# Performance work log

Hardware: AMD Instinct MI355X
Metric: run time of the kernel (lower is better)

Reference implementation:

```python
import jax, jax.numpy as jnp
import numpy as np
import math

BLOCK_SIZE = 512

def _block_attention(query, key, value):
    # query/key/value: [B, S, H, D]; block-wise attention with PER-BLOCK softmax
    # and normalizer accumulation, faithful to _ring_attention_single (causal, no dropout).
    B, S, H, D = query.shape
    bs = BLOCK_SIZE
    nb = S // bs
    scale = 1.0 / math.sqrt(D)
    neg = jnp.where(jnp.triu(jnp.ones((bs, bs), dtype=bool), 1), -jnp.inf, 0.0)  # strict-upper causal mask for diagonal block
    outs = []
    for i in range(nb):  # small fixed number of blocks (8)
        qb = query[:, i * bs:(i + 1) * bs]                      # [B, bs, H, D]
        kb = key[:, :(i + 1) * bs]                              # [B, (i+1)*bs, H, D]
        vb = value[:, :(i + 1) * bs].reshape(B, i + 1, bs, H, D)
        s = jnp.einsum('bqhd,bkhd->bhqk', qb, kb) * scale       # [B, H, bs, (i+1)*bs]
        s = s.reshape(B, H, bs, i + 1, bs)
        s = s.at[:, :, :, i, :].add(neg)                        # causal mask on diagonal block j == i
        p = jax.nn.softmax(s, axis=-1)                          # softmax PER kv block (faithful to source)
        o = jnp.einsum('bhqjk,bjkhd->bqhd', p, vb)              # accumulated block outputs
        norm = p.sum(axis=-1).sum(axis=-1)                      # [B, H, bs] accumulated normalizer (== i+1 per row)
        norm = jnp.clip(norm, 1e-6, None).transpose(0, 2, 1)[..., None]  # [B, bs, H, 1]
        outs.append(o / norm)
    return jnp.concatenate(outs, axis=1)  # [B, S, H, D]


def setup_inputs() -> dict:
    key = jax.random.key(0)
    k1, k2, k3 = jax.random.split(key, 3)
    shape = (2, 4096, 16, 128)
    return {
        'query': jax.random.normal(k1, shape, dtype=jnp.float32),
        'key': jax.random.normal(k2, shape, dtype=jnp.float32),
        'value': jax.random.normal(k3, shape, dtype=jnp.float32),
    }


def reference(query, key, value):
    return _block_attention(query, key, value)
```

## Files before the change

### kernel.cpp

```cpp
#include <hip/hip_runtime.h>

typedef short bf16x8 __attribute__((ext_vector_type(8)));
typedef short bf16x4 __attribute__((ext_vector_type(4)));
typedef float f32x4  __attribute__((ext_vector_type(4)));
typedef float f32x16 __attribute__((ext_vector_type(16)));
typedef unsigned int u32;
typedef u32 u32x4 __attribute__((ext_vector_type(4)));

#define SEQ 4096
#define NH  16
#define HD  128

__device__ __forceinline__ short bf16_rne(float x) {
  u32 u = __builtin_bit_cast(u32, x);
  u = (u + 0x7FFFu + ((u >> 16) & 1u)) >> 16;
  return (short)u;
}

typedef __attribute__((address_space(1))) const void as1c_void;
typedef __attribute__((address_space(3))) void as3_void;

#define CVTPK(d, a, b) asm("v_cvt_pk_bf16_f32 %0, %1, %2" : "=v"(d) : "v"(a), "v"(b))
#define PLSWAP(x, y)   asm("v_permlane32_swap_b32 %0, %1" : "+v"(x), "+v"(y))

__global__ __launch_bounds__(256) void prep_k(const float* __restrict__ K,
                                              short* __restrict__ Kp) {
  int idx = blockIdx.x * 256 + threadIdx.x;
  int d4 = idx & 31;
  int s  = (idx >> 5) & 4095;
  int h  = (idx >> 17) & 15;
  int b  = idx >> 21;
  f32x4 v = *(const f32x4*)(K + (((size_t)(b * SEQ + s) * NH + h) << 7) + d4 * 4);
  bf16x4 o;
  o[0] = bf16_rne(v[0]); o[1] = bf16_rne(v[1]);
  o[2] = bf16_rne(v[2]); o[3] = bf16_rne(v[3]);
  int x = (d4 * 4) ^ ((s & 7) << 3);
  *(bf16x4*)(Kp + (((size_t)(b * NH + h) * SEQ + s) << 7) + x) = o;
}

__global__ __launch_bounds__(256) void prep_v(const float* __restrict__ V,
                                              short* __restrict__ Vt) {
  __shared__ short tile[64 * 128];
  int bid = blockIdx.x;
  int sb = bid & 63;
  int h  = (bid >> 6) & 15;
  int b  = bid >> 10;
  int t = threadIdx.x;
  {
    int s = t >> 2;
    int dbase = (t & 3) * 32;
    const float* src = V + (((size_t)(b * SEQ + sb * 64 + s) * NH + h) << 7) + dbase;
    int sw = (s & 7) << 3;
#pragma unroll
    for (int j = 0; j < 8; ++j) {
      f32x4 v = *(const f32x4*)(src + j * 4);
      bf16x4 o;
      o[0] = bf16_rne(v[0]); o[1] = bf16_rne(v[1]);
      o[2] = bf16_rne(v[2]); o[3] = bf16_rne(v[3]);
      int d = dbase + j * 4;
      *(bf16x4*)&tile[s * 128 + (d ^ sw)] = o;
    }
  }
  __syncthreads();
  {
    int w = t >> 6, l = t & 63, g = l >> 4, lq = l & 15;
    int srel = lq * 4;
#pragma unroll
    for (int j = 0; j < 8; ++j) {
      int d = w * 32 + j * 4 + g;
      bf16x4 o;
#pragma unroll
      for (int i = 0; i < 4; ++i) {
        int s = srel + i;
        o[i] = tile[s * 128 + (d ^ ((s & 7) << 3))];
      }
      int sp = srel ^ ((d & 7) << 3);
      *(bf16x4*)(Vt + (((size_t)(b * NH + h) * HD + d) << 12) + sb * 64 + sp) = o;
    }
  }
}

__global__ __launch_bounds__(256, 2) void attn_main(const float* __restrict__ Q,
                                                    const short* __restrict__ Kp,
                                                    const short* __restrict__ Vt,
                                                    float* __restrict__ Out) {
  __shared__ __align__(16) short sK[2][64 * 128];
  __shared__ __align__(16) short sV[2][128 * 64];

  int bid0 = (int)blockIdx.x;
  int bid = (bid0 & 7) * 64 + (bid0 >> 3);
  int p  = bid & 15;
  int h  = (bid >> 4) & 15;
  int b  = bid >> 8;

  int tid = threadIdx.x;
  int l = tid & 63, w = tid >> 6;
  int q5 = l & 31;
  int hi = l >> 5;
  int hi4 = hi * 4, hi8 = hi * 8;
  int cswz = (l & 7) << 4;

  int kcol[8], vcol[4];
#pragma unroll
  for (int i = 0; i < 8; ++i) kcol[i] = (i * 32 + hi * 16) ^ cswz;
#pragma unroll
  for (int ks = 0; ks < 4; ++ks) vcol[ks] = (ks * 32 + hi * 16) ^ cswz;

  const int pat[16] = {0,1,2,3, 8,9,10,11, 16,17,18,19, 24,25,26,27};

  const char* KbB = (const char*)(Kp + ((size_t)(b * NH + h) << 19));
  const char* VbB = (const char*)(Vt + ((size_t)(b * NH + h) << 19));

  const char* kgb[4]; const char* vgb[4]; int ldo[4];
#pragma unroll
  for (int j = 0; j < 4; ++j) {
    int idx = j * 256 + tid;
    kgb[j] = KbB + idx * 16;
    vgb[j] = VbB + (size_t)(idx >> 3) * 8192 + (idx & 7) * 16;
    ldo[j] = idx * 16;
  }

  const float SCL = 0.08838834764831845f * 1.4426950408889634f;

  for (int ts = 0; ts < 2; ++ts) {
    int qt = ts ? p : (31 - p);
    int iblk = qt >> 2;
    int qrow0 = qt * 128 + w * 32;
    int qg = qrow0 + q5;
    int qgrel = (qt & 3) * 128 + w * 32 + q5;
    int nch_w = (qt & 3) * 2 + (w >> 1) + 1;
    int ntot = 8 * iblk + (qt & 3) * 2 + 2;

    bf16x8 qf[8];
    {
      const float* qp = Q + (((size_t)(b * SEQ + qg) * NH + h) << 7);
#pragma unroll
      for (int i = 0; i < 8; ++i) {
        int d0 = i * 16 + hi8;
        f32x4 a = *(const f32x4*)(qp + d0);
        f32x4 c2 = *(const f32x4*)(qp + d0 + 4);
        bf16x8 f;
        f[0] = bf16_rne(a[0] * SCL);  f[1] = bf16_rne(a[1] * SCL);
        f[2] = bf16_rne(a[2] * SCL);  f[3] = bf16_rne(a[3] * SCL);
        f[4] = bf16_rne(c2[0] * SCL); f[5] = bf16_rne(c2[1] * SCL);
        f[6] = bf16_rne(c2[2] * SCL); f[7] = bf16_rne(c2[3] * SCL);
        qf[i] = f;
      }
    }

    f32x16 ot[4], ob[4];
#pragma unroll
    for (int dt = 0; dt < 4; ++dt) {
#pragma unroll
      for (int r = 0; r < 16; ++r) { ot[dt][r] = 0.f; ob[dt][r] = 0.f; }
    }
    float Z = 0.0f;

    __syncthreads();
#pragma unroll
    for (int j = 0; j < 4; ++j) {
      __builtin_amdgcn_global_load_lds((as1c_void*)kgb[j], (as3_void*)((char*)sK[0] + ldo[j]), 16, 0, 0);
      __builtin_amdgcn_global_load_lds((as1c_void*)vgb[j], (as3_void*)((char*)sV[0] + ldo[j]), 16, 0, 0);
    }

#pragma unroll 2
    for (int t = 0; t < ntot; ++t) {
      __syncthreads();

      int bi = (t + 1) & 1;
      if (t + 1 < ntot) {
#pragma unroll
        for (int j = 0; j < 4; ++j) {
          __builtin_amdgcn_global_load_lds((as1c_void*)(kgb[j] + (size_t)(t + 1) * 16384),
                                           (as3_void*)((char*)sK[bi] + ldo[j]), 16, 0, 0);
          __builtin_amdgcn_global_load_lds((as1c_void*)(vgb[j] + (size_t)(t + 1) * 128),
                                           (as3_void*)((char*)sV[bi] + ldo[j]), 16, 0, 0);
        }
      }

      int jb = t >> 3, c = t & 7;
      const int diag = (jb == iblk);

      if (!(diag && c >= nch_w)) {
        const char* kbuf = (const char*)sK[t & 1];
        const char* vbuf = (const char*)sV[t & 1];
        float csum = 0.0f;

        f32x16 st0, st1;
#pragma unroll
        for (int r = 0; r < 16; ++r) { st0[r] = 0.f; st1[r] = 0.f; }
        int rowb = q5 * 256;
        __builtin_amdgcn_s_setprio(1);
#pragma unroll
        for (int i = 0; i < 8; ++i) {
          bf16x8 kf0 = *(const bf16x8*)(kbuf + rowb + kcol[i]);
          bf16x8 kf1 = *(const bf16x8*)(kbuf + 8192 + rowb + kcol[i]);
          st0 = __builtin_amdgcn_mfma_f32_32x32x16_bf16(kf0, qf[i], st0, 0, 0, 0);
          st1 = __builtin_amdgcn_mfma_f32_32x32x16_bf16(kf1, qf[i], st1, 0, 0, 0);
        }
        __builtin_amdgcn_s_setprio(0);

        if (diag && c == nch_w - 1) {
          int lim0 = qgrel - c * 64;
          int lim1 = lim0 - 32;
#pragma unroll
          for (int r = 0; r < 16; ++r) {
            int pr4 = pat[r] + hi4;
            if (pr4 > lim0) st0[r] = -1e30f;
            if (pr4 > lim1) st1[r] = -1e30f;
          }
        }

        bf16x8 pa0, pa1, pa2, pa3;
        {
          float pr[16];
#pragma unroll
          for (int r = 0; r < 16; ++r) {
            pr[r] = __builtin_amdgcn_exp2f(st0[r]);
            csum += pr[r];
          }
          u32 X0, X1, Y0, Y1, A0, A1, B0, B1;
          CVTPK(X0, pr[0], pr[1]);   CVTPK(X1, pr[2], pr[3]);
          CVTPK(Y0, pr[4], pr[5]);   CVTPK(Y1, pr[6], pr[7]);
          PLSWAP(X0, Y0); PLSWAP(X1, Y1);
          pa0 = __builtin_bit_cast(bf16x8, (u32x4){X0, X1, Y0, Y1});
          CVTPK(A0, pr[8], pr[9]);   CVTPK(A1, pr[10], pr[11]);
          CVTPK(B0, pr[12], pr[13]); CVTPK(B1, pr[14], pr[15]);
          PLSWAP(A0, B0); PLSWAP(A1, B1);
          pa1 = __builtin_bit_cast(bf16x8, (u32x4){A0, A1, B0, B1});
        }
        __builtin_amdgcn_s_setprio(1);
#pragma unroll
        for (int dt = 0; dt < 4; ++dt) {
          bf16x8 vf = *(const bf16x8*)(vbuf + (dt * 32 + q5) * 128 + vcol[0]);
          ob[dt] = __builtin_amdgcn_mfma_f32_32x32x16_bf16(pa0, vf, ob[dt], 0, 0, 0);
        }
#pragma unroll
        for (int dt = 0; dt < 4; ++dt) {
          bf16x8 vf = *(const bf16x8*)(vbuf + (dt * 32 + q5) * 128 + vcol[1]);
          ob[dt] = __builtin_amdgcn_mfma_f32_32x32x16_bf16(pa1, vf, ob[dt], 0, 0, 0);
        }
        __builtin_amdgcn_s_setprio(0);

        {
          float pr[16];
#pragma unroll
          for (int r = 0; r < 16; ++r) {
            pr[r] = __builtin_amdgcn_exp2f(st1[r]);
            csum += pr[r];
          }
          u32 X0, X1, Y0, Y1, A0, A1, B0, B1;
          CVTPK(X0, pr[0], pr[1]);   CVTPK(X1, pr[2], pr[3]);
          CVTPK(Y0, pr[4], pr[5]);   CVTPK(Y1, pr[6], pr[7]);
          PLSWAP(X0, Y0); PLSWAP(X1, Y1);
          pa2 = __builtin_bit_cast(bf16x8, (u32x4){X0, X1, Y0, Y1});
          CVTPK(A0, pr[8], pr[9]);   CVTPK(A1, pr[10], pr[11]);
          CVTPK(B0, pr[12], pr[13]); CVTPK(B1, pr[14], pr[15]);
          PLSWAP(A0, B0); PLSWAP(A1, B1);
          pa3 = __builtin_bit_cast(bf16x8, (u32x4){A0, A1, B0, B1});
        }
        __builtin_amdgcn_s_setprio(1);
#pragma unroll
        for (int dt = 0; dt < 4; ++dt) {
          bf16x8 vf = *(const bf16x8*)(vbuf + (dt * 32 + q5) * 128 + vcol[2]);
          ob[dt] = __builtin_amdgcn_mfma_f32_32x32x16_bf16(pa2, vf, ob[dt], 0, 0, 0);
        }
#pragma unroll
        for (int dt = 0; dt < 4; ++dt) {
          bf16x8 vf = *(const bf16x8*)(vbuf + (dt * 32 + q5) * 128 + vcol[3]);
          ob[dt] = __builtin_amdgcn_mfma_f32_32x32x16_bf16(pa3, vf, ob[dt], 0, 0, 0);
        }
        __builtin_amdgcn_s_setprio(0);

        Z += csum;
      }

      if ((t & 7) == 7 || t == ntot - 1) {
        float zf = Z + __shfl_xor(Z, 32, 64);
        float rzL = 1.0f / zf;
        float rz[16];
#pragma unroll
        for (int r = 0; r < 16; ++r) rz[r] = __shfl(rzL, pat[r] + hi4, 64);
#pragma unroll
        for (int dt = 0; dt < 4; ++dt) {
#pragma unroll
          for (int r = 0; r < 16; ++r) {
            ot[dt][r] += ob[dt][r] * rz[r];
            ob[dt][r] = 0.f;
          }
        }
        Z = 0.0f;
      }
    }

    float rnorm = 1.0f / (float)(iblk + 1);
#pragma unroll
    for (int dt = 0; dt < 4; ++dt) {
#pragma unroll
      for (int r = 0; r < 16; ++r) {
        int qrow = qrow0 + pat[r] + hi4;
        Out[(((size_t)(b * SEQ + qrow) * NH + h) << 7) + dt * 32 + q5] = ot[dt][r] * rnorm;
      }
    }
  }
}

extern "C" void kernel_launch(void* const* d_in, const int* in_sizes, int n_in,
                              void* d_out, int out_size, void* d_ws, size_t ws_size,
                              hipStream_t stream) {
  const float* Q = (const float*)d_in[0];
  const float* K = (const float*)d_in[1];
  const float* V = (const float*)d_in[2];
  float* out = (float*)d_out;

  short* Kp = (short*)d_ws;
  short* Vt = Kp + (size_t)2 * NH * SEQ * HD;

  prep_k<<<(2 * NH * SEQ * (HD / 4)) / 256, 256, 0, stream>>>(K, Kp);
  prep_v<<<2 * NH * (SEQ / 64), 256, 0, stream>>>(V, Vt);
  attn_main<<<2 * NH * 16, 256, 0, stream>>>(Q, Kp, Vt, out);
}
```

Baseline: 206.6 us.

## Software-pipeline PV of previous tile with QK of current tile

Restructures the KV loop so each iteration runs the QK^T MFMAs for the current tile, then the P·V MFMAs for the previous tile's probabilities, then the softmax/exp for the current tile. This interleaves independent matrix work with exp and conversion work to hide latency. V staging becomes triple-buffered so the previous tile's V stays resident while the next one loads, and the block-normalizer fold is deferred to follow the matching PV. In exchange it raises LDS use to 80 KB per block and register pressure, since the probability fragments are carried across iterations, and it drops the unroll-2 pragma.

```diff
diff --git a/kernel.cpp b/kernel.cpp
--- a/kernel.cpp
+++ b/kernel.cpp
@@ -85,7 +85,7 @@
                                                     const short* __restrict__ Vt,
                                                     float* __restrict__ Out) {
   __shared__ __align__(16) short sK[2][64 * 128];
-  __shared__ __align__(16) short sV[2][128 * 64];
+  __shared__ __align__(16) short sV[3][128 * 64];
 
   int bid0 = (int)blockIdx.x;
   int bid = (bid0 & 7) * 64 + (bid0 >> 3);
@@ -156,51 +156,98 @@
     }
     float Z = 0.0f;
 
+    char* kcur = (char*)&sK[0][0]; char* knxt = (char*)&sK[1][0];
+    char* vcur = (char*)&sV[0][0]; char* vnxt = (char*)&sV[1][0]; char* vfre = (char*)&sV[2][0];
+
     __syncthreads();
 #pragma unroll
     for (int j = 0; j < 4; ++j) {
-      __builtin_amdgcn_global_load_lds((as1c_void*)kgb[j], (as3_void*)((char*)sK[0] + ldo[j]), 16, 0, 0);
-      __builtin_amdgcn_global_load_lds((as1c_void*)vgb[j], (as3_void*)((char*)sV[0] + ldo[j]), 16, 0, 0);
-    }
-
-#pragma unroll 2
+      __builtin_amdgcn_global_load_lds((as1c_void*)kgb[j], (as3_void*)(kcur + ldo[j]), 16, 0, 0);
+      __builtin_amdgcn_global_load_lds((as1c_void*)vgb[j], (as3_void*)(vcur + ldo[j]), 16, 0, 0);
+    }
+
+    bf16x8 pa0p, pa1p, pa2p, pa3p;
+    const char* pvb = vcur;
+    int havepa = 0, foldafter = 0;
+    f32x16 st0, st1;
+
+    auto QK = [&]() {
+#pragma unroll
+      for (int r = 0; r < 16; ++r) { st0[r] = 0.f; st1[r] = 0.f; }
+      int rowb = q5 * 256;
+      __builtin_amdgcn_s_setprio(1);
+#pragma unroll
+      for (int i = 0; i < 8; ++i) {
+        bf16x8 kf0 = *(const bf16x8*)(kcur + rowb + kcol[i]);
+        bf16x8 kf1 = *(const bf16x8*)(kcur + 8192 + rowb + kcol[i]);
+        st0 = __builtin_amdgcn_mfma_f32_32x32x16_bf16(kf0, qf[i], st0, 0, 0, 0);
+        st1 = __builtin_amdgcn_mfma_f32_32x32x16_bf16(kf1, qf[i], st1, 0, 0, 0);
+      }
+      __builtin_amdgcn_s_setprio(0);
+    };
+    auto PV = [&]() {
+      __builtin_amdgcn_s_setprio(1);
+#pragma unroll
+      for (int dt = 0; dt < 4; ++dt) {
+        bf16x8 vf = *(const bf16x8*)(pvb + (dt * 32 + q5) * 128 + vcol[0]);
+        ob[dt] = __builtin_amdgcn_mfma_f32_32x32x16_bf16(pa0p, vf, ob[dt], 0, 0, 0);
+      }
+#pragma unroll
+      for (int dt = 0; dt < 4; ++dt) {
+        bf16x8 vf = *(const bf16x8*)(pvb + (dt * 32 + q5) * 128 + vcol[1]);
+        ob[dt] = __builtin_amdgcn_mfma_f32_32x32x16_bf16(pa1p, vf, ob[dt], 0, 0, 0);
+      }
+#pragma unroll
+      for (int dt = 0; dt < 4; ++dt) {
+        bf16x8 vf = *(const bf16x8*)(pvb + (dt * 32 + q5) * 128 + vcol[2]);
+        ob[dt] = __builtin_amdgcn_mfma_f32_32x32x16_bf16(pa2p, vf, ob[dt], 0, 0, 0);
+      }
+#pragma unroll
+      for (int dt = 0; dt < 4; ++dt) {
+        bf16x8 vf = *(const bf16x8*)(pvb + (dt * 32 + q5) * 128 + vcol[3]);
+        ob[dt] = __builtin_amdgcn_mfma_f32_32x32x16_bf16(pa3p, vf, ob[dt], 0, 0, 0);
+      }
+      __builtin_amdgcn_s_setprio(0);
+    };
+    auto FOLD = [&]() {
+      float zf = Z + __shfl_xor(Z, 32, 64);
+      float rzL = 1.0f / zf;
+      float rz[16];
+#pragma unroll
+      for (int r = 0; r < 16; ++r) rz[r] = __shfl(rzL, pat[r] + hi4, 64);
+#pragma unroll
+      for (int dt = 0; dt < 4; ++dt) {
+#pragma unroll
+        for (int r = 0; r < 16; ++r) {
+          ot[dt][r] += ob[dt][r] * rz[r];
+          ob[dt][r] = 0.f;
+        }
+      }
+      Z = 0.0f;
+    };
+
     for (int t = 0; t < ntot; ++t) {
       __syncthreads();
 
-      int bi = (t + 1) & 1;
       if (t + 1 < ntot) {
 #pragma unroll
         for (int j = 0; j < 4; ++j) {
           __builtin_amdgcn_global_load_lds((as1c_void*)(kgb[j] + (size_t)(t + 1) * 16384),
-                                           (as3_void*)((char*)sK[bi] + ldo[j]), 16, 0, 0);
+                                           (as3_void*)(knxt + ldo[j]), 16, 0, 0);
           __builtin_amdgcn_global_load_lds((as1c_void*)(vgb[j] + (size_t)(t + 1) * 128),
-                                           (as3_void*)((char*)sV[bi] + ldo[j]), 16, 0, 0);
+                                           (as3_void*)(vnxt + ldo[j]), 16, 0, 0);
         }
       }
 
       int jb = t >> 3, c = t & 7;
-      const int diag = (jb == iblk);
-
-      if (!(diag && c >= nch_w)) {
-        const char* kbuf = (const char*)sK[t & 1];
-        const char* vbuf = (const char*)sV[t & 1];
-        float csum = 0.0f;
-
-        f32x16 st0, st1;
-#pragma unroll
-        for (int r = 0; r < 16; ++r) { st0[r] = 0.f; st1[r] = 0.f; }
-        int rowb = q5 * 256;
-        __builtin_amdgcn_s_setprio(1);
-#pragma unroll
-        for (int i = 0; i < 8; ++i) {
-          bf16x8 kf0 = *(const bf16x8*)(kbuf + rowb + kcol[i]);
-          bf16x8 kf1 = *(const bf16x8*)(kbuf + 8192 + rowb + kcol[i]);
-          st0 = __builtin_amdgcn_mfma_f32_32x32x16_bf16(kf0, qf[i], st0, 0, 0, 0);
-          st1 = __builtin_amdgcn_mfma_f32_32x32x16_bf16(kf1, qf[i], st1, 0, 0, 0);
-        }
-        __builtin_amdgcn_s_setprio(0);
-
-        if (diag && c == nch_w - 1) {
+      int contrib = !(jb == iblk && c >= nch_w);
+
+      bf16x8 na0, na1, na2, na3;
+      float csum = 0.0f;
+      int nfold = (jb < iblk) ? (c == 7) : (c == nch_w - 1);
+
+      auto SM = [&]() {
+        if (jb == iblk && c == nch_w - 1) {
           int lim0 = qgrel - c * 64;
           int lim1 = lim0 - 32;
 #pragma unroll
@@ -210,87 +257,66 @@
             if (pr4 > lim1) st1[r] = -1e30f;
           }
         }
-
-        bf16x8 pa0, pa1, pa2, pa3;
         {
           float pr[16];
 #pragma unroll
-          for (int r = 0; r < 16; ++r) {
-            pr[r] = __builtin_amdgcn_exp2f(st0[r]);
-            csum += pr[r];
-          }
+          for (int r = 0; r < 16; ++r) { pr[r] = __builtin_amdgcn_exp2f(st0[r]); csum += pr[r]; }
           u32 X0, X1, Y0, Y1, A0, A1, B0, B1;
           CVTPK(X0, pr[0], pr[1]);   CVTPK(X1, pr[2], pr[3]);
           CVTPK(Y0, pr[4], pr[5]);   CVTPK(Y1, pr[6], pr[7]);
           PLSWAP(X0, Y0); PLSWAP(X1, Y1);
-          pa0 = __builtin_bit_cast(bf16x8, (u32x4){X0, X1, Y0, Y1});
+          na0 = __builtin_bit_cast(bf16x8, (u32x4){X0, X1, Y0, Y1});
           CVTPK(A0, pr[8], pr[9]);   CVTPK(A1, pr[10], pr[11]);
           CVTPK(B0, pr[12], pr[13]); CVTPK(B1, pr[14], pr[15]);
           PLSWAP(A0, B0); PLSWAP(A1, B1);
-          pa1 = __builtin_bit_cast(bf16x8, (u32x4){A0, A1, B0, B1});
-        }
-        __builtin_amdgcn_s_setprio(1);
-#pragma unroll
-        for (int dt = 0; dt < 4; ++dt) {
-          bf16x8 vf = *(const bf16x8*)(vbuf + (dt * 32 + q5) * 128 + vcol[0]);
-          ob[dt] = __builtin_amdgcn_mfma_f32_32x32x16_bf16(pa0, vf, ob[dt], 0, 0, 0);
-        }
-#pragma unroll
-        for (int dt = 0; dt < 4; ++dt) {
-          bf16x8 vf = *(const bf16x8*)(vbuf + (dt * 32 + q5) * 128 + vcol[1]);
-          ob[dt] = __builtin_amdgcn_mfma_f32_32x32x16_bf16(pa1, vf, ob[dt], 0, 0, 0);
-        }
-        __builtin_amdgcn_s_setprio(0);
-
+          na1 = __builtin_bit_cast(bf16x8, (u32x4){A0, A1, B0, B1});
+        }
         {
           float pr[16];
 #pragma unroll
-          for (int r = 0; r < 16; ++r) {
-            pr[r] = __builtin_amdgcn_exp2f(st1[r]);
-            csum += pr[r];
-          }
+          for (int r = 0; r < 16; ++r) { pr[r] = __builtin_amdgcn_exp2f(st1[r]); csum += pr[r]; }
           u32 X0, X1, Y0, Y1, A0, A1, B0, B1;
           CVTPK(X0, pr[0], pr[1]);   CVTPK(X1, pr[2], pr[3]);
           CVTPK(Y0, pr[4], pr[5]);   CVTPK(Y1, pr[6], pr[7]);
           PLSWAP(X0, Y0); PLSWAP(X1, Y1);
-          pa2 = __builtin_bit_cast(bf16x8, (u32x4){X0, X1, Y0, Y1});
+          na2 = __builtin_bit_cast(bf16x8, (u32x4){X0, X1, Y0, Y1});
           CVTPK(A0, pr[8], pr[9]);   CVTPK(A1, pr[10], pr[11]);
           CVTPK(B0, pr[12], pr[13]); CVTPK(B1, pr[14], pr[15]);
           PLSWAP(A0, B0); PLSWAP(A1, B1);
-          pa3 = __builtin_bit_cast(bf16x8, (u32x4){A0, A1, B0, B1});
-        }
-        __builtin_amdgcn_s_setprio(1);
-#pragma unroll
-        for (int dt = 0; dt < 4; ++dt) {
-          bf16x8 vf = *(const bf16x8*)(vbuf + (dt * 32 + q5) * 128 + vcol[2]);
-          ob[dt] = __builtin_amdgcn_mfma_f32_32x32x16_bf16(pa2, vf, ob[dt], 0, 0, 0);
-        }
-#pragma unroll
-        for (int dt = 0; dt < 4; ++dt) {
-          bf16x8 vf = *(const bf16x8*)(vbuf + (dt * 32 + q5) * 128 + vcol[3]);
-          ob[dt] = __builtin_amdgcn_mfma_f32_32x32x16_bf16(pa3, vf, ob[dt], 0, 0, 0);
-        }
-        __builtin_amdgcn_s_setprio(0);
-
+          na3 = __builtin_bit_cast(bf16x8, (u32x4){A0, A1, B0, B1});
+        }
+      };
+
+      if (contrib && havepa) {
+        QK();
+        PV();
+        SM();
+        if (foldafter) FOLD();
+      } else if (contrib) {
+        QK();
+        SM();
+      } else if (havepa) {
+        PV();
+        if (foldafter) FOLD();
+      }
+
+      if (contrib) {
         Z += csum;
-      }
-
-      if ((t & 7) == 7 || t == ntot - 1) {
-        float zf = Z + __shfl_xor(Z, 32, 64);
-        float rzL = 1.0f / zf;
-        float rz[16];
-#pragma unroll
-        for (int r = 0; r < 16; ++r) rz[r] = __shfl(rzL, pat[r] + hi4, 64);
-#pragma unroll
-        for (int dt = 0; dt < 4; ++dt) {
-#pragma unroll
-          for (int r = 0; r < 16; ++r) {
-            ot[dt][r] += ob[dt][r] * rz[r];
-            ob[dt][r] = 0.f;
-          }
-        }
-        Z = 0.0f;
-      }
+        pa0p = na0; pa1p = na1; pa2p = na2; pa3p = na3;
+        pvb = vcur;
+        foldafter = nfold;
+        havepa = 1;
+      } else {
+        havepa = 0;
+      }
+
+      { char* tk = kcur; kcur = knxt; knxt = tk; }
+      { char* tv = vcur; vcur = vnxt; vnxt = vfre; vfre = tv; }
+    }
+
+    if (havepa) {
+      PV();
+      FOLD();
     }
 
     float rnorm = 1.0f / (float)(iblk + 1);
```

Measured after the change: 234.6 us. +13.5%, slower.

## Pack output accumulator as bf16 pairs and split QK MFMA chains

Applied to the files above, without the earlier changes.

The cross-block output accumulator moves from 64 fp32 registers to 32 packed-bf16 registers to lower register pressure. The QK^T MFMA chain is split into two independent accumulators per tile so that dependent MFMAs can overlap, and the row-sum reduction is split into four partial sums. The s_setprio hints are removed. Accumulating the output in bf16 across eight blocks loses precision, and the extra accumulators add registers elsewhere.

```diff
diff --git a/kernel.cpp b/kernel.cpp
--- a/kernel.cpp
+++ b/kernel.cpp
@@ -6,6 +6,7 @@
 typedef float f32x16 __attribute__((ext_vector_type(16)));
 typedef unsigned int u32;
 typedef u32 u32x4 __attribute__((ext_vector_type(4)));
+typedef u32 u32x16 __attribute__((ext_vector_type(16)));
 
 #define SEQ 4096
 #define NH  16
@@ -22,6 +23,13 @@
 
 #define CVTPK(d, a, b) asm("v_cvt_pk_bf16_f32 %0, %1, %2" : "=v"(d) : "v"(a), "v"(b))
 #define PLSWAP(x, y)   asm("v_permlane32_swap_b32 %0, %1" : "+v"(x), "+v"(y))
+
+__device__ __forceinline__ float bflo(u32 u) {
+  return __builtin_bit_cast(float, u << 16);
+}
+__device__ __forceinline__ float bfhi(u32 u) {
+  return __builtin_bit_cast(float, u & 0xFFFF0000u);
+}
 
 __global__ __launch_bounds__(256) void prep_k(const float* __restrict__ K,
                                               short* __restrict__ Kp) {
@@ -148,11 +156,14 @@
       }
     }
 
-    f32x16 ot[4], ob[4];
+    u32x16 otp[2];
+    f32x16 ob[4];
+#pragma unroll
+    for (int r = 0; r < 16; ++r) { otp[0][r] = 0u; otp[1][r] = 0u; }
 #pragma unroll
     for (int dt = 0; dt < 4; ++dt) {
 #pragma unroll
-      for (int r = 0; r < 16; ++r) { ot[dt][r] = 0.f; ob[dt][r] = 0.f; }
+      for (int r = 0; r < 16; ++r) ob[dt][r] = 0.f;
     }
     float Z = 0.0f;
 
@@ -184,21 +195,26 @@
       if (!(diag && c >= nch_w)) {
         const char* kbuf = (const char*)sK[t & 1];
         const char* vbuf = (const char*)sV[t & 1];
-        float csum = 0.0f;
-
+        float c0 = 0.f, c1 = 0.f, c2s = 0.f, c3 = 0.f;
+
+        f32x16 s0a, s0b, s1a, s1b;
+#pragma unroll
+        for (int r = 0; r < 16; ++r) { s0a[r] = 0.f; s0b[r] = 0.f; s1a[r] = 0.f; s1b[r] = 0.f; }
+        int rowb = q5 * 256;
+#pragma unroll
+        for (int i = 0; i < 4; ++i) {
+          bf16x8 kf0a = *(const bf16x8*)(kbuf + rowb + kcol[i]);
+          bf16x8 kf1a = *(const bf16x8*)(kbuf + 8192 + rowb + kcol[i]);
+          bf16x8 kf0b = *(const bf16x8*)(kbuf + rowb + kcol[i + 4]);
+          bf16x8 kf1b = *(const bf16x8*)(kbuf + 8192 + rowb + kcol[i + 4]);
+          s0a = __builtin_amdgcn_mfma_f32_32x32x16_bf16(kf0a, qf[i], s0a, 0, 0, 0);
+          s1a = __builtin_amdgcn_mfma_f32_32x32x16_bf16(kf1a, qf[i], s1a, 0, 0, 0);
+          s0b = __builtin_amdgcn_mfma_f32_32x32x16_bf16(kf0b, qf[i + 4], s0b, 0, 0, 0);
+          s1b = __builtin_amdgcn_mfma_f32_32x32x16_bf16(kf1b, qf[i + 4], s1b, 0, 0, 0);
+        }
         f32x16 st0, st1;
 #pragma unroll
-        for (int r = 0; r < 16; ++r) { st0[r] = 0.f; st1[r] = 0.f; }
-        int rowb = q5 * 256;
-        __builtin_amdgcn_s_setprio(1);
-#pragma unroll
-        for (int i = 0; i < 8; ++i) {
-          bf16x8 kf0 = *(const bf16x8*)(kbuf + rowb + kcol[i]);
-          bf16x8 kf1 = *(const bf16x8*)(kbuf + 8192 + rowb + kcol[i]);
-          st0 = __builtin_amdgcn_mfma_f32_32x32x16_bf16(kf0, qf[i], st0, 0, 0, 0);
-          st1 = __builtin_amdgcn_mfma_f32_32x32x16_bf16(kf1, qf[i], st1, 0, 0, 0);
-        }
-        __builtin_amdgcn_s_setprio(0);
+        for (int r = 0; r < 16; ++r) { st0[r] = s0a[r] + s0b[r]; st1[r] = s1a[r] + s1b[r]; }
 
         if (diag && c == nch_w - 1) {
           int lim0 = qgrel - c * 64;
@@ -215,10 +231,11 @@
         {
           float pr[16];
 #pragma unroll
-          for (int r = 0; r < 16; ++r) {
-            pr[r] = __builtin_amdgcn_exp2f(st0[r]);
-            csum += pr[r];
-          }
+          for (int r = 0; r < 16; ++r) pr[r] = __builtin_amdgcn_exp2f(st0[r]);
+          c0 += pr[0] + pr[4];  c1 += pr[1] + pr[5];
+          c2s += pr[2] + pr[6]; c3 += pr[3] + pr[7];
+          c0 += pr[8] + pr[12]; c1 += pr[9] + pr[13];
+          c2s += pr[10] + pr[14]; c3 += pr[11] + pr[15];
           u32 X0, X1, Y0, Y1, A0, A1, B0, B1;
           CVTPK(X0, pr[0], pr[1]);   CVTPK(X1, pr[2], pr[3]);
           CVTPK(Y0, pr[4], pr[5]);   CVTPK(Y1, pr[6], pr[7]);
@@ -229,7 +246,6 @@
           PLSWAP(A0, B0); PLSWAP(A1, B1);
           pa1 = __builtin_bit_cast(bf16x8, (u32x4){A0, A1, B0, B1});
         }
-        __builtin_amdgcn_s_setprio(1);
 #pragma unroll
         for (int dt = 0; dt < 4; ++dt) {
           bf16x8 vf = *(const bf16x8*)(vbuf + (dt * 32 + q5) * 128 + vcol[0]);
@@ -240,15 +256,15 @@
           bf16x8 vf = *(const bf16x8*)(vbuf + (dt * 32 + q5) * 128 + vcol[1]);
           ob[dt] = __builtin_amdgcn_mfma_f32_32x32x16_bf16(pa1, vf, ob[dt], 0, 0, 0);
         }
-        __builtin_amdgcn_s_setprio(0);
 
         {
           float pr[16];
 #pragma unroll
-          for (int r = 0; r < 16; ++r) {
-            pr[r] = __builtin_amdgcn_exp2f(st1[r]);
-            csum += pr[r];
-          }
+          for (int r = 0; r < 16; ++r) pr[r] = __builtin_amdgcn_exp2f(st1[r]);
+          c0 += pr[0] + pr[4];  c1 += pr[1] + pr[5];
+          c2s += pr[2] + pr[6]; c3 += pr[3] + pr[7];
+          c0 += pr[8] + pr[12]; c1 += pr[9] + pr[13];
+          c2s += pr[10] + pr[14]; c3 += pr[11] + pr[15];
           u32 X0, X1, Y0, Y1, A0, A1, B0, B1;
           CVTPK(X0, pr[0], pr[1]);   CVTPK(X1, pr[2], pr[3]);
           CVTPK(Y0, pr[4], pr[5]);   CVTPK(Y1, pr[6], pr[7]);
@@ -259,7 +275,6 @@
           PLSWAP(A0, B0); PLSWAP(A1, B1);
           pa3 = __builtin_bit_cast(bf16x8, (u32x4){A0, A1, B0, B1});
         }
-        __builtin_amdgcn_s_setprio(1);
 #pragma unroll
         for (int dt = 0; dt < 4; ++dt) {
           bf16x8 vf = *(const bf16x8*)(vbuf + (dt * 32 + q5) * 128 + vcol[2]);
@@ -270,9 +285,8 @@
           bf16x8 vf = *(const bf16x8*)(vbuf + (dt * 32 + q5) * 128 + vcol[3]);
           ob[dt] = __builtin_amdgcn_mfma_f32_32x32x16_bf16(pa3, vf, ob[dt], 0, 0, 0);
         }
-        __builtin_amdgcn_s_setprio(0);
-
-        Z += csum;
+
+        Z += (c0 + c1) + (c2s + c3);
       }
 
       if ((t & 7) == 7 || t == ntot - 1) {
@@ -282,11 +296,14 @@
 #pragma unroll
         for (int r = 0; r < 16; ++r) rz[r] = __shfl(rzL, pat[r] + hi4, 64);
 #pragma unroll
-        for (int dt = 0; dt < 4; ++dt) {
+        for (int j = 0; j < 2; ++j) {
 #pragma unroll
           for (int r = 0; r < 16; ++r) {
-            ot[dt][r] += ob[dt][r] * rz[r];
-            ob[dt][r] = 0.f;
+            float lo = bflo(otp[j][r]) + ob[2 * j][r] * rz[r];
+            float hh = bfhi(otp[j][r]) + ob[2 * j + 1][r] * rz[r];
+            CVTPK(otp[j][r], lo, hh);
+            ob[2 * j][r] = 0.f;
+            ob[2 * j + 1][r] = 0.f;
           }
         }
         Z = 0.0f;
@@ -295,11 +312,13 @@
 
     float rnorm = 1.0f / (float)(iblk + 1);
 #pragma unroll
-    for (int dt = 0; dt < 4; ++dt) {
+    for (int j = 0; j < 2; ++j) {
 #pragma unroll
       for (int r = 0; r < 16; ++r) {
         int qrow = qrow0 + pat[r] + hi4;
-        Out[(((size_t)(b * SEQ + qrow) * NH + h) << 7) + dt * 32 + q5] = ot[dt][r] * rnorm;
+        size_t base = (((size_t)(b * SEQ + qrow) * NH + h) << 7) + q5;
+        Out[base + (2 * j) * 32] = bflo(otp[j][r]) * rnorm;
+        Out[base + (2 * j + 1) * 32] = bfhi(otp[j][r]) * rnorm;
       }
     }
   }
```

After: 213.7 us. +3.4%, slower.
